# Kernel tuning notes

Measured on AMD Instinct MI355X. Metric: run time of the kernel, lower is better.

Reference implementation:

```python
import jax, jax.numpy as jnp
import numpy as np

H = 16
ATTN_TEMP = 1.5
CLS_TEMP = 2.0


def setup_inputs() -> dict:
    key = jax.random.key(0)
    ks = jax.random.split(key, 11)
    B, Nq, Nk, C = 2, 2048, 2048, 1024
    x_q = jax.random.normal(ks[0], (B, Nq, C), jnp.float32)
    x_kv = jax.random.normal(ks[1], (B, Nk, C), jnp.float32)
    cls_token = jax.random.normal(ks[2], (B, 1, C), jnp.float32)
    s = 0.02
    Wq = jax.random.normal(ks[3], (C, C), jnp.float32) * s
    bq = jax.random.normal(ks[4], (C,), jnp.float32) * s
    Wk = jax.random.normal(ks[5], (C, C), jnp.float32) * s
    bk = jax.random.normal(ks[6], (C,), jnp.float32) * s
    Wv = jax.random.normal(ks[7], (C, C), jnp.float32) * s
    bv = jax.random.normal(ks[8], (C,), jnp.float32) * s
    Wp = jax.random.normal(ks[9], (C, C), jnp.float32) * s
    bp = jax.random.normal(ks[10], (C,), jnp.float32) * s
    return {"x_q": x_q, "x_kv": x_kv, "cls_token": cls_token,
            "Wq": Wq, "bq": bq, "Wk": Wk, "bk": bk, "Wv": Wv, "bv": bv,
            "Wp": Wp, "bp": bp}


def reference(x_q, x_kv, cls_token, Wq, bq, Wk, bk, Wv, bv, Wp, bp):
    B, Nq, C = x_q.shape
    Nk = x_kv.shape[1]
    Dh = C // H
    scale = Dh ** -0.5
    # torch Linear: y = x @ W.T + b, W is [out, in]
    q = (x_q @ Wq.T + bq).reshape(B, Nq, H, Dh).transpose(0, 2, 1, 3)   # [B,H,Nq,Dh]
    k = (x_kv @ Wk.T + bk).reshape(B, Nk, H, Dh).transpose(0, 2, 1, 3)  # [B,H,Nk,Dh]
    v = (x_kv @ Wv.T + bv).reshape(B, Nk, H, Dh).transpose(0, 2, 1, 3)  # [B,H,Nk,Dh]
    attn_logits = jnp.einsum('bhqd,bhkd->bhqk', q, k) * (scale / ATTN_TEMP)
    # cls-token affinity mask: raw cls_token (NOT passed through q-proj)
    cls_tok = cls_token.reshape(B, 1, H, Dh).transpose(0, 2, 1, 3)      # [B,H,1,Dh]
    aff = jax.nn.sigmoid(jnp.einsum('bhqd,bhkd->bhqk', cls_tok, k) * (scale / CLS_TEMP))
    aff = aff.mean(axis=1, keepdims=True)                               # [B,1,1,Nk]
    m = aff.min(axis=-1, keepdims=True)
    M = aff.max(axis=-1, keepdims=True)
    aff_mask = (aff - m) / (M - m + 1e-6)
    attn = jax.nn.softmax(attn_logits, axis=-1) * aff_mask              # [B,H,Nq,Nk]
    x = jnp.einsum('bhqk,bhkd->bqhd', attn, v).reshape(B, Nq, C)
    x = x @ Wp.T + bp
    return (x, attn_logits.sum(axis=1) / H, aff_mask)
```

## Files before the change

kernel.cpp:

```cpp
#include <hip/hip_runtime.h>
#include <stdint.h>
#include <math.h>

typedef unsigned short u16;
typedef __attribute__((ext_vector_type(8))) short bh8;
typedef __attribute__((ext_vector_type(4))) float f32x4;
typedef __attribute__((ext_vector_type(16))) float f32x16;

#define MFMA16(a,b,c) __builtin_amdgcn_mfma_f32_16x16x32_bf16((a),(b),(c),0,0,0)
#define MFMA32(a,b,c) __builtin_amdgcn_mfma_f32_32x32x16_bf16((a),(b),(c),0,0,0)

__device__ __forceinline__ int swz3(int r){ return (r ^ (r >> 3)) & 7; }

__device__ __forceinline__ u16 f2bf(float f){
  union { float f; uint32_t i; } x; x.f = f;
  uint32_t r = x.i + 0x7fffu + ((x.i >> 16) & 1u);
  return (u16)(r >> 16);
}
__device__ __forceinline__ float bf2f(u16 u){
  union { uint32_t i; float f; } x; x.i = ((uint32_t)u) << 16; return x.f;
}
__device__ __forceinline__ uint32_t cvtpk(float a, float b){
  uint32_t r;
  asm("v_cvt_pk_bf16_f32 %0, %1, %2" : "=v"(r) : "v"(a), "v"(b));
  return r;
}
__device__ __forceinline__ float fexp2(float x){
  float r; asm("v_exp_f32 %0, %1" : "=v"(r) : "v"(x)); return r;
}

__device__ __forceinline__ void gld16(void* lds, const void* g){
  __builtin_amdgcn_global_load_lds(
      (__attribute__((address_space(1))) unsigned int*)const_cast<void*>(g),
      (__attribute__((address_space(3))) unsigned int*)lds, 16, 0, 0);
}

__global__ __launch_bounds__(256) void cvt_all_kernel(
    const float* __restrict__ xq, const float* __restrict__ xkv,
    const float* __restrict__ Wq, const float* __restrict__ Wk,
    const float* __restrict__ Wv, const float* __restrict__ Wp,
    u16* __restrict__ oxq, u16* __restrict__ oxkv,
    u16* __restrict__ oWq, u16* __restrict__ oWk,
    u16* __restrict__ oWv, u16* __restrict__ oWp,
    int nx8, int nw8)
{
  int i = blockIdx.x * 256 + threadIdx.x;
  const float* s; u16* d; int o;
  if (i < 2 * nx8){
    if (i < nx8){ s = xq; d = oxq; o = i; }
    else        { s = xkv; d = oxkv; o = i - nx8; }
  } else {
    int k = i - 2 * nx8;
    if (k >= 4 * nw8) return;
    int wsel = k / nw8; o = k - wsel * nw8;
    s = (wsel == 0) ? Wq : (wsel == 1) ? Wk : (wsel == 2) ? Wv : Wp;
    d = (wsel == 0) ? oWq : (wsel == 1) ? oWk : (wsel == 2) ? oWv : oWp;
  }
  const float4* sp = (const float4*)s + 2 * (size_t)o;
  float4 a = sp[0], b = sp[1];
  bh8 r;
  r[0]=(short)f2bf(a.x); r[1]=(short)f2bf(a.y); r[2]=(short)f2bf(a.z); r[3]=(short)f2bf(a.w);
  r[4]=(short)f2bf(b.x); r[5]=(short)f2bf(b.y); r[6]=(short)f2bf(b.z); r[7]=(short)f2bf(b.w);
  *(bh8*)(d + (size_t)o * 8) = r;
}

template<bool OUT_BF16, bool HAS_BIAS>
__device__ __forceinline__ void gemm_body(
    const u16* __restrict__ A, const u16* __restrict__ Bm,
    const float* __restrict__ bias, void* __restrict__ outp,
    int N, int K, int bm, int bn, float scale,
    u16* As, u16* Bs)
{
  const int tid = threadIdx.x, lane = tid & 63, w = tid >> 6;
  const int wm = w >> 1, wn = w & 1;
  const int l15 = lane & 15, l4 = lane >> 4;
  f32x4 acc[4][4];
  const f32x4 vz = {0.f, 0.f, 0.f, 0.f};
  #pragma unroll
  for (int m = 0; m < 4; ++m)
    #pragma unroll
    for (int n = 0; n < 4; ++n) acc[m][n] = vz;

  const u16* Arow = A + (size_t)bm * K;
  const u16* Brow = Bm + (size_t)bn * K;
  const int nkt = K >> 6;
  for (int kt = 0; kt < nkt; ++kt){
    #pragma unroll
    for (int it = 0; it < 4; ++it){
      int cb = w * 256 + it * 64;
      int c = cb + lane;
      int j = c >> 3;
      int dd = (c & 7) ^ swz3(j);
      gld16(&As[cb * 8], Arow + (size_t)j * K + kt * 64 + dd * 8);
      gld16(&Bs[cb * 8], Brow + (size_t)j * K + kt * 64 + dd * 8);
    }
    __syncthreads();
    #pragma unroll
    for (int s = 0; s < 2; ++s){
      bh8 af[4], bfr[4];
      #pragma unroll
      for (int m = 0; m < 4; ++m){
        int row = wm * 64 + m * 16 + l15;
        af[m] = *(const bh8*)&As[row * 64 + (((s * 4 + l4) ^ swz3(row)) << 3)];
      }
      #pragma unroll
      for (int n = 0; n < 4; ++n){
        int row = wn * 64 + n * 16 + l15;
        bfr[n] = *(const bh8*)&Bs[row * 64 + (((s * 4 + l4) ^ swz3(row)) << 3)];
      }
      #pragma unroll
      for (int m = 0; m < 4; ++m)
        #pragma unroll
        for (int n = 0; n < 4; ++n)
          acc[m][n] = MFMA16(af[m], bfr[n], acc[m][n]);
    }
    __syncthreads();
  }
  #pragma unroll
  for (int m = 0; m < 4; ++m){
    int row0 = bm + wm * 64 + m * 16 + l4 * 4;
    #pragma unroll
    for (int n = 0; n < 4; ++n){
      int col = bn + wn * 64 + n * 16 + l15;
      float bv = HAS_BIAS ? bias[col] : 0.f;
      #pragma unroll
      for (int r = 0; r < 4; ++r){
        float v = (acc[m][n][r] + bv) * scale;
        size_t idx = (size_t)(row0 + r) * N + col;
        if (OUT_BF16) ((u16*)outp)[idx] = f2bf(v);
        else          ((float*)outp)[idx] = v;
      }
    }
  }
}

__global__ __launch_bounds__(256) void proj_gemm_kernel(
    const u16* __restrict__ xq, const u16* __restrict__ xkv,
    const u16* __restrict__ Wq, const u16* __restrict__ Wk, const u16* __restrict__ Wv,
    const float* __restrict__ bq, const float* __restrict__ bk, const float* __restrict__ bv,
    u16* __restrict__ Q, u16* __restrict__ Ko, u16* __restrict__ V, float qscale)
{
  __shared__ __align__(16) u16 As[128 * 64];
  __shared__ __align__(16) u16 Bs[128 * 64];
  int z = blockIdx.z;
  const u16* A   = (z == 0) ? xq : xkv;
  const u16* W   = (z == 0) ? Wq : (z == 1) ? Wk : Wv;
  const float* b = (z == 0) ? bq : (z == 1) ? bk : bv;
  u16* out       = (z == 0) ? Q  : (z == 1) ? Ko : V;
  float sc       = (z == 0) ? qscale : 1.0f;
  gemm_body<true, true>(A, W, b, out, 1024, 1024,
                        blockIdx.y * 128, blockIdx.x * 128, sc, As, Bs);
}

__global__ __launch_bounds__(256) void out1_gemm_kernel(
    const u16* __restrict__ Q, const u16* __restrict__ Kb,
    float* __restrict__ out1, int Nq, int Nk, float scale)
{
  __shared__ __align__(16) u16 As[128 * 64];
  __shared__ __align__(16) u16 Bs[128 * 64];
  int b = blockIdx.z;
  gemm_body<false, false>(Q + (size_t)b * Nq * 1024, Kb + (size_t)b * Nk * 1024,
                          nullptr, out1 + (size_t)b * Nq * Nk, Nk, 1024,
                          blockIdx.y * 128, blockIdx.x * 128, scale, As, Bs);
}

__global__ __launch_bounds__(256) void out0_gemm_kernel(
    const u16* __restrict__ X, const u16* __restrict__ Wp,
    const float* __restrict__ bp, float* __restrict__ out)
{
  __shared__ __align__(16) u16 As[128 * 64];
  __shared__ __align__(16) u16 Bs[128 * 64];
  gemm_body<false, true>(X, Wp, bp, out, 1024, 1024,
                         blockIdx.y * 128, blockIdx.x * 128, 1.0f, As, Bs);
}

__global__ __launch_bounds__(256) void aff_kernel(
    const float* __restrict__ cls, const u16* __restrict__ Kb,
    float* __restrict__ aff, int Nk)
{
  int lane = threadIdx.x & 63;
  int gw = (blockIdx.x * 256 + threadIdx.x) >> 6;
  int b = gw / Nk, j = gw - b * Nk;
  const u16* kr = Kb + ((size_t)(b * Nk + j)) * 1024;
  const float* c = cls + (size_t)b * 1024;
  float total = 0.f;
  #pragma unroll
  for (int half = 0; half < 2; ++half){
    int d0 = half * 512 + lane * 8;
    bh8 kv = *(const bh8*)(kr + d0);
    float4 ca = *(const float4*)(c + d0);
    float4 cb = *(const float4*)(c + d0 + 4);
    float p = bf2f((u16)kv[0]) * ca.x + bf2f((u16)kv[1]) * ca.y
            + bf2f((u16)kv[2]) * ca.z + bf2f((u16)kv[3]) * ca.w
            + bf2f((u16)kv[4]) * cb.x + bf2f((u16)kv[5]) * cb.y
            + bf2f((u16)kv[6]) * cb.z + bf2f((u16)kv[7]) * cb.w;
    p += __shfl_xor(p, 1); p += __shfl_xor(p, 2); p += __shfl_xor(p, 4);
    float sig = 1.f / (1.f + __expf(-0.0625f * p));
    total += sig;
  }
  total += __shfl_xor(total, 8); total += __shfl_xor(total, 16); total += __shfl_xor(total, 32);
  if (lane == 0) aff[gw] = total * (1.0f / 128.0f);
}

__global__ __launch_bounds__(1024) void affnorm_kernel(
    const float* __restrict__ aff, float* __restrict__ mask,
    float* __restrict__ out2, int Nk)
{
  int b = blockIdx.x, tid = threadIdx.x;
  const float* a = aff + (size_t)b * Nk;
  float mn = 1e30f, mx = -1e30f;
  for (int i = tid; i < Nk; i += 1024){
    float v = a[i]; mn = fminf(mn, v); mx = fmaxf(mx, v);
  }
  #pragma unroll
  for (int off = 1; off < 64; off <<= 1){
    mn = fminf(mn, __shfl_xor(mn, off));
    mx = fmaxf(mx, __shfl_xor(mx, off));
  }
  __shared__ float smn[16], smx[16];
  int wv = tid >> 6;
  if ((tid & 63) == 0){ smn[wv] = mn; smx[wv] = mx; }
  __syncthreads();
  mn = smn[tid & 15]; mx = smx[tid & 15];
  #pragma unroll
  for (int off = 1; off < 16; off <<= 1){
    mn = fminf(mn, __shfl_xor(mn, off));
    mx = fmaxf(mx, __shfl_xor(mx, off));
  }
  float inv = 1.f / ((mx - mn) + 1e-6f);
  for (int i = tid; i < Nk; i += 1024){
    float v = (a[i] - mn) * inv;
    mask[(size_t)b * Nk + i] = v;
    out2[(size_t)b * Nk + i] = v;
  }
}

__global__ __launch_bounds__(256) void vtrans_kernel(
    const u16* __restrict__ Vb, const float* __restrict__ affm,
    u16* __restrict__ Vtg, int Nk)
{
  __shared__ u16 T[64][72];
  int t0 = blockIdx.x * 64, h = blockIdx.y, b = blockIdx.z;
  int tid = threadIdx.x;
  int row = tid & 63, cp = tid >> 6;
  const u16* src = Vb + ((size_t)(b * Nk) + t0 + row) * 1024 + h * 64 + cp * 16;
  *(bh8*)&T[row][cp * 16]     = *(const bh8*)(src);
  *(bh8*)&T[row][cp * 16 + 8] = *(const bh8*)(src + 8);
  __syncthreads();
  int d = tid >> 2, kc = (tid & 3) * 16;
  const float* av = affm + (size_t)b * Nk + t0 + kc;
  u16* dst = Vtg + ((size_t)(b * 16 + h) * 64 + d) * 2048 + t0 + kc;
  bh8 o0, o1;
  #pragma unroll
  for (int j = 0; j < 8; ++j)
    o0[j] = (short)f2bf(bf2f(T[kc + j][d]) * av[j]);
  #pragma unroll
  for (int j = 0; j < 8; ++j)
    o1[j] = (short)f2bf(bf2f(T[kc + 8 + j][d]) * av[8 + j]);
  *(bh8*)dst = o0;
  *(bh8*)(dst + 8) = o1;
}

__global__ __launch_bounds__(256, 4) void flash_kernel(
    const u16* __restrict__ Qb, const u16* __restrict__ Kb, const u16* __restrict__ Vtg,
    u16* __restrict__ Opart, float* __restrict__ Lpart, int Nq, int Nk, int nqb, int perx)
{
  __shared__ __align__(16) u16 Ks[2][64 * 64];
  __shared__ __align__(16) u16 Vs[2][64 * 64];
  const int tid = threadIdx.x, lane = tid & 63, w = tid >> 6;
  const int l31 = lane & 31, hi = lane >> 5;

  int bid = blockIdx.x;
  int xcd = bid & 7, slot = bid >> 3;
  int spg = nqb * 2;
  int gl = slot / spg;
  int within = slot - gl * spg;
  int g = xcd * perx + gl;
  int qb = within >> 1, sp = within & 1;
  int h = g & 15, b = g >> 4;
  int q0 = qb * 128;

  const u16* Qg = Qb + ((size_t)b * Nq + q0 + w * 32 + l31) * 1024 + h * 64;
  const u16* Kg = Kb + ((size_t)b * Nk) * 1024 + h * 64;
  const u16* Vg = Vtg + ((size_t)(b * 16 + h)) * 64 * (size_t)Nk;

  bh8 qf[4];
  #pragma unroll
  for (int s = 0; s < 4; ++s)
    qf[s] = *(const bh8*)(Qg + s * 16 + hi * 8);

  union { short s[8]; bh8 v; } one8;
  #pragma unroll
  for (int j = 0; j < 8; ++j) one8.s[j] = (short)0x3F80;
  const bh8 onesf = one8.v;

  f32x16 O0, O1, Lacc;
  #pragma unroll
  for (int r = 0; r < 16; ++r){ O0[r] = 0.f; O1[r] = 0.f; Lacc[r] = 0.f; }
  f32x16 z16;
  #pragma unroll
  for (int r = 0; r < 16; ++r) z16[r] = 0.f;

  const int tpers = (Nk >> 6) >> 1;
  const int t0 = sp * tpers;

  #define STAGE(T, PB) do {                                                    \
    int t_ = (T);                                                              \
    _Pragma("unroll")                                                          \
    for (int it = 0; it < 2; ++it){                                            \
      int cb = (w * 2 + it) * 64;                                              \
      int c = cb + lane;                                                       \
      int j = c >> 3, dd = (c & 7) ^ swz3(j);                                  \
      gld16(&Ks[PB][cb * 8], Kg + (size_t)(t_ * 64 + j) * 1024 + dd * 8);      \
      gld16(&Vs[PB][cb * 8], Vg + (size_t)j * Nk + t_ * 64 + dd * 8);          \
    }                                                                          \
  } while (0)

  STAGE(t0, 0);
  __syncthreads();

  for (int ti = 0; ti < tpers; ++ti){
    int pb = ti & 1;
    if (ti + 1 < tpers) STAGE(t0 + ti + 1, pb ^ 1);

    f32x16 S0, S1;
    #pragma unroll
    for (int s = 0; s < 4; ++s){
      bh8 kf0 = *(const bh8*)&Ks[pb][l31 * 64 + (((s * 2 + hi) ^ swz3(l31)) << 3)];
      bh8 kf1 = *(const bh8*)&Ks[pb][(32 + l31) * 64 + (((s * 2 + hi) ^ swz3(32 + l31)) << 3)];
      if (s == 0){
        S0 = MFMA32(kf0, qf[0], z16);
        S1 = MFMA32(kf1, qf[0], z16);
      } else {
        S0 = MFMA32(kf0, qf[s], S0);
        S1 = MFMA32(kf1, qf[s], S1);
      }
    }

    #pragma unroll
    for (int r = 0; r < 16; ++r) S0[r] = fexp2(S0[r]);
    #pragma unroll
    for (int r = 0; r < 16; ++r) S1[r] = fexp2(S1[r]);

    bh8 pa[4];
    #pragma unroll
    for (int ks = 0; ks < 4; ++ks){
      int r0 = (ks & 1) * 8;
      float p0, p1, p2, p3, p4, p5, p6, p7;
      if (ks < 2){ p0=S0[r0]; p1=S0[r0+1]; p2=S0[r0+2]; p3=S0[r0+3];
                   p4=S0[r0+4]; p5=S0[r0+5]; p6=S0[r0+6]; p7=S0[r0+7]; }
      else       { p0=S1[r0]; p1=S1[r0+1]; p2=S1[r0+2]; p3=S1[r0+3];
                   p4=S1[r0+4]; p5=S1[r0+5]; p6=S1[r0+6]; p7=S1[r0+7]; }
      uint32_t x0 = cvtpk(p0, p1), x1 = cvtpk(p2, p3);
      uint32_t y0 = cvtpk(p4, p5), y1 = cvtpk(p6, p7);
      asm volatile("v_permlane32_swap_b32 %0, %1" : "+v"(x0), "+v"(y0));
      asm volatile("v_permlane32_swap_b32 %0, %1" : "+v"(x1), "+v"(y1));
      union { uint32_t u[4]; bh8 v; } pk;
      pk.u[0] = x0; pk.u[1] = x1; pk.u[2] = y0; pk.u[3] = y1;
      pa[ks] = pk.v;
    }

    #pragma unroll
    for (int ks = 0; ks < 4; ++ks){
      bh8 vf0 = *(const bh8*)&Vs[pb][l31 * 64 + (((ks * 2 + hi) ^ swz3(l31)) << 3)];
      bh8 vf1 = *(const bh8*)&Vs[pb][(32 + l31) * 64 + (((ks * 2 + hi) ^ swz3(32 + l31)) << 3)];
      O0 = MFMA32(pa[ks], vf0, O0);
      O1 = MFMA32(pa[ks], vf1, O1);
      Lacc = MFMA32(pa[ks], onesf, Lacc);
    }
    __syncthreads();
  }
  #undef STAGE

  size_t gs = (size_t)(g * 2 + sp);
  #pragma unroll
  for (int r = 0; r < 16; ++r){
    int qc = (r & 3) + 8 * (r >> 2);
    int qrow = q0 + w * 32 + qc + 4 * hi;
    size_t base = (gs * Nq + qrow) * 64;
    Opart[base + l31]      = f2bf(O0[r]);
    Opart[base + 32 + l31] = f2bf(O1[r]);
    if (l31 == 0) Lpart[gs * Nq + qrow] = Lacc[r];
  }
}

__global__ __launch_bounds__(256) void combine_kernel(
    const u16* __restrict__ Opart, const float* __restrict__ Lpart,
    u16* __restrict__ xo, int Nq)
{
  int i = blockIdx.x * 256 + threadIdx.x;
  int g = i >> 14;
  int rem = i & 16383;
  int q = rem >> 3, dc = (rem & 7) << 3;
  size_t ba = (((size_t)g * 2 + 0) * Nq + q) * 64 + dc;
  size_t bb = (((size_t)g * 2 + 1) * Nq + q) * 64 + dc;
  float la = Lpart[((size_t)g * 2 + 0) * Nq + q];
  float lb = Lpart[((size_t)g * 2 + 1) * Nq + q];
  float inv = 1.f / (la + lb);
  bh8 av = *(const bh8*)(Opart + ba);
  bh8 bv = *(const bh8*)(Opart + bb);
  int b_ = g >> 4, h = g & 15;
  u16* dst = xo + ((size_t)b_ * Nq + q) * 1024 + h * 64 + dc;
  bh8 o;
  #pragma unroll
  for (int j = 0; j < 8; ++j)
    o[j] = (short)f2bf((bf2f((u16)av[j]) + bf2f((u16)bv[j])) * inv);
  *(bh8*)dst = o;
}

extern "C" void kernel_launch(void* const* d_in, const int* in_sizes, int n_in,
                              void* d_out, int out_size, void* d_ws, size_t ws_size,
                              hipStream_t stream)
{
  const float* x_q  = (const float*)d_in[0];
  const float* x_kv = (const float*)d_in[1];
  const float* cls  = (const float*)d_in[2];
  const float* bq   = (const float*)d_in[4];
  const float* bk   = (const float*)d_in[6];
  const float* bv   = (const float*)d_in[8];
  const float* bp   = (const float*)d_in[10];
  const float* Wq   = (const float*)d_in[3];
  const float* Wk   = (const float*)d_in[5];
  const float* Wv   = (const float*)d_in[7];
  const float* Wp   = (const float*)d_in[9];

  const int Nq = 2048, Nk = 2048, C = 1024;
  const int B = in_sizes[0] / (Nq * C);
  const size_t nX = (size_t)B * Nq * C;
  const size_t nW = (size_t)C * C;

  char* wsb = (char*)d_ws;
  size_t off = 0;
  auto alloc = [&](size_t bytes) -> char* {
    char* p = wsb + off; off += (bytes + 255) & ~(size_t)255; return p;
  };
  u16* xqb  = (u16*)alloc(nX * 2);
  u16* xkvb = (u16*)alloc(nX * 2);
  u16* Wqb  = (u16*)alloc(nW * 2);
  u16* Wkb  = (u16*)alloc(nW * 2);
  u16* Wvb  = (u16*)alloc(nW * 2);
  u16* Wpb  = (u16*)alloc(nW * 2);
  u16* Qb   = (u16*)alloc(nX * 2);
  u16* Kb   = (u16*)alloc(nX * 2);
  u16* Vb   = (u16*)alloc(nX * 2);
  u16* Vtg  = (u16*)alloc(nX * 2);
  u16* Xat  = (u16*)alloc(nX * 2);
  float* aff   = (float*)alloc((size_t)B * Nk * 4);
  float* affm  = (float*)alloc((size_t)B * Nk * 4);
  u16*   Opart = xqb;
  float* Lpart = (float*)Wqb;

  float* out0 = (float*)d_out;
  float* out1 = out0 + (size_t)B * Nq * C;
  float* out2 = out1 + (size_t)B * Nq * Nk;

  int nx8 = (int)(nX / 8), nw8 = (int)(nW / 8);
  int total = 2 * nx8 + 4 * nw8;
  cvt_all_kernel<<<(total + 255) / 256, 256, 0, stream>>>(
      x_q, x_kv, Wq, Wk, Wv, Wp, xqb, xkvb, Wqb, Wkb, Wvb, Wpb, nx8, nw8);

  const float c2 = (0.125f / 1.5f) * 1.44269504088896f;
  proj_gemm_kernel<<<dim3(C / 128, (B * Nq) / 128, 3), 256, 0, stream>>>(
      xqb, xkvb, Wqb, Wkb, Wvb, bq, bk, bv, Qb, Kb, Vb, c2);

  aff_kernel<<<(B * Nk) / 4, 256, 0, stream>>>(cls, Kb, aff, Nk);
  affnorm_kernel<<<B, 1024, 0, stream>>>(aff, affm, out2, Nk);

  vtrans_kernel<<<dim3(Nk / 64, 16, B), 256, 0, stream>>>(Vb, affm, Vtg, Nk);

  const float c1s = (0.125f / (1.5f * 16.f)) / c2;
  out1_gemm_kernel<<<dim3(Nk / 128, Nq / 128, B), 256, 0, stream>>>(
      Qb, Kb, out1, Nq, Nk, c1s);

  int nqb = Nq / 128;
  int perx = (16 * B) / 8;
  flash_kernel<<<dim3(nqb * 16 * B * 2), 256, 0, stream>>>(
      Qb, Kb, Vtg, Opart, Lpart, Nq, Nk, nqb, perx);

  combine_kernel<<<(16 * B * Nq * 8) / 256, 256, 0, stream>>>(Opart, Lpart, Xat, Nq);

  out0_gemm_kernel<<<dim3(C / 128, (B * Nq) / 128, 1), 256, 0, stream>>>(
      Xat, Wpb, bp, out0);
}
```

Baseline: 269.4 us.

## Double-buffer GEMM LDS tiles and raise wave priority around MFMA blocks

The shared GEMM body now uses two LDS buffers per operand and prefetches the next K-tile with async global-to-LDS loads while MFMAs run on the current tile, which removes one barrier per iteration. s_setprio is raised around the MFMA clusters in both the GEMM and the attention kernel so waves issuing matrix ops get scheduling preference. The cost is doubled LDS per block (64 KB), which can lower occupancy. The prefetch also relies on the single trailing barrier to make the next stage visible.

```diff
diff --git a/kernel.cpp b/kernel.cpp
--- a/kernel.cpp
+++ b/kernel.cpp
@@ -84,38 +84,51 @@
   const u16* Arow = A + (size_t)bm * K;
   const u16* Brow = Bm + (size_t)bn * K;
   const int nkt = K >> 6;
+
+  #define GSTAGE(KT, PB) do {                                                  \
+    int kt_ = (KT);                                                            \
+    _Pragma("unroll")                                                          \
+    for (int it = 0; it < 4; ++it){                                            \
+      int cb = w * 256 + it * 64;                                              \
+      int c = cb + lane;                                                       \
+      int j = c >> 3;                                                          \
+      int dd = (c & 7) ^ swz3(j);                                              \
+      gld16(&As[(PB) * 8192 + cb * 8], Arow + (size_t)j * K + kt_ * 64 + dd * 8); \
+      gld16(&Bs[(PB) * 8192 + cb * 8], Brow + (size_t)j * K + kt_ * 64 + dd * 8); \
+    }                                                                          \
+  } while (0)
+
+  GSTAGE(0, 0);
+  __syncthreads();
+
   for (int kt = 0; kt < nkt; ++kt){
-    #pragma unroll
-    for (int it = 0; it < 4; ++it){
-      int cb = w * 256 + it * 64;
-      int c = cb + lane;
-      int j = c >> 3;
-      int dd = (c & 7) ^ swz3(j);
-      gld16(&As[cb * 8], Arow + (size_t)j * K + kt * 64 + dd * 8);
-      gld16(&Bs[cb * 8], Brow + (size_t)j * K + kt * 64 + dd * 8);
-    }
-    __syncthreads();
+    int pb = kt & 1;
+    if (kt + 1 < nkt) GSTAGE(kt + 1, pb ^ 1);
     #pragma unroll
     for (int s = 0; s < 2; ++s){
       bh8 af[4], bfr[4];
       #pragma unroll
       for (int m = 0; m < 4; ++m){
         int row = wm * 64 + m * 16 + l15;
-        af[m] = *(const bh8*)&As[row * 64 + (((s * 4 + l4) ^ swz3(row)) << 3)];
+        af[m] = *(const bh8*)&As[pb * 8192 + row * 64 + (((s * 4 + l4) ^ swz3(row)) << 3)];
       }
       #pragma unroll
       for (int n = 0; n < 4; ++n){
         int row = wn * 64 + n * 16 + l15;
-        bfr[n] = *(const bh8*)&Bs[row * 64 + (((s * 4 + l4) ^ swz3(row)) << 3)];
+        bfr[n] = *(const bh8*)&Bs[pb * 8192 + row * 64 + (((s * 4 + l4) ^ swz3(row)) << 3)];
       }
+      __builtin_amdgcn_s_setprio(1);
       #pragma unroll
       for (int m = 0; m < 4; ++m)
         #pragma unroll
         for (int n = 0; n < 4; ++n)
           acc[m][n] = MFMA16(af[m], bfr[n], acc[m][n]);
+      __builtin_amdgcn_s_setprio(0);
     }
     __syncthreads();
   }
+  #undef GSTAGE
+
   #pragma unroll
   for (int m = 0; m < 4; ++m){
     int row0 = bm + wm * 64 + m * 16 + l4 * 4;
@@ -140,8 +153,8 @@
     const float* __restrict__ bq, const float* __restrict__ bk, const float* __restrict__ bv,
     u16* __restrict__ Q, u16* __restrict__ Ko, u16* __restrict__ V, float qscale)
 {
-  __shared__ __align__(16) u16 As[128 * 64];
-  __shared__ __align__(16) u16 Bs[128 * 64];
+  __shared__ __align__(16) u16 As[2 * 128 * 64];
+  __shared__ __align__(16) u16 Bs[2 * 128 * 64];
   int z = blockIdx.z;
   const u16* A   = (z == 0) ? xq : xkv;
   const u16* W   = (z == 0) ? Wq : (z == 1) ? Wk : Wv;
@@ -156,8 +169,8 @@
     const u16* __restrict__ Q, const u16* __restrict__ Kb,
     float* __restrict__ out1, int Nq, int Nk, float scale)
 {
-  __shared__ __align__(16) u16 As[128 * 64];
-  __shared__ __align__(16) u16 Bs[128 * 64];
+  __shared__ __align__(16) u16 As[2 * 128 * 64];
+  __shared__ __align__(16) u16 Bs[2 * 128 * 64];
   int b = blockIdx.z;
   gemm_body<false, false>(Q + (size_t)b * Nq * 1024, Kb + (size_t)b * Nk * 1024,
                           nullptr, out1 + (size_t)b * Nq * Nk, Nk, 1024,
@@ -168,8 +181,8 @@
     const u16* __restrict__ X, const u16* __restrict__ Wp,
     const float* __restrict__ bp, float* __restrict__ out)
 {
-  __shared__ __align__(16) u16 As[128 * 64];
-  __shared__ __align__(16) u16 Bs[128 * 64];
+  __shared__ __align__(16) u16 As[2 * 128 * 64];
+  __shared__ __align__(16) u16 Bs[2 * 128 * 64];
   gemm_body<false, true>(X, Wp, bp, out, 1024, 1024,
                          blockIdx.y * 128, blockIdx.x * 128, 1.0f, As, Bs);
 }
@@ -324,6 +337,7 @@
     if (ti + 1 < tpers) STAGE(t0 + ti + 1, pb ^ 1);
 
     f32x16 S0, S1;
+    __builtin_amdgcn_s_setprio(1);
     #pragma unroll
     for (int s = 0; s < 4; ++s){
       bh8 kf0 = *(const bh8*)&Ks[pb][l31 * 64 + (((s * 2 + hi) ^ swz3(l31)) << 3)];
@@ -336,6 +350,7 @@
         S1 = MFMA32(kf1, qf[s], S1);
       }
     }
+    __builtin_amdgcn_s_setprio(0);
 
     #pragma unroll
     for (int r = 0; r < 16; ++r) S0[r] = fexp2(S0[r]);
@@ -360,6 +375,7 @@
       pa[ks] = pk.v;
     }
 
+    __builtin_amdgcn_s_setprio(1);
     #pragma unroll
     for (int ks = 0; ks < 4; ++ks){
       bh8 vf0 = *(const bh8*)&Vs[pb][l31 * 64 + (((ks * 2 + hi) ^ swz3(l31)) << 3)];
@@ -368,6 +384,7 @@
       O1 = MFMA32(pa[ks], vf1, O1);
       Lacc = MFMA32(pa[ks], onesf, Lacc);
     }
+    __builtin_amdgcn_s_setprio(0);
     __syncthreads();
   }
   #undef STAGE
```

Result: no change. 273.8 us (+1.6%).
